# Optimization experiments

Hardware: AMD Instinct MI355X
Metric: run time of the kernel (lower is better)

Reference implementation:

```python
import jax, jax.numpy as jnp
import numpy as np

HID = 128
OUT = 1
L = 4
N_NODES = 50000
N_EDGES = 600000
NUM_GRAPHS = 256
ATOM_FEATS, ATOM_VOCAB = 9, 64
BOND_FEATS, BOND_VOCAB = 3, 8
BN_EPS = 1e-5


def setup_inputs() -> dict:
    key = jax.random.key(0)
    ks = jax.random.split(key, 16)
    x = jax.random.randint(ks[0], (N_NODES, ATOM_FEATS), 0, ATOM_VOCAB)
    edge_index = jax.random.randint(ks[1], (2, N_EDGES), 0, N_NODES)
    edge_attr = jax.random.randint(ks[2], (N_EDGES, BOND_FEATS), 0, BOND_VOCAB)
    batch = jnp.sort(jax.random.randint(ks[3], (N_NODES,), 0, NUM_GRAPHS))
    s = 0.05
    atom_emb = jax.random.normal(ks[4], (ATOM_FEATS, ATOM_VOCAB, HID), jnp.float32) * s
    bond_emb = jax.random.normal(ks[5], (BOND_FEATS, BOND_VOCAB, HID), jnp.float32) * s
    lin1_w = jax.random.normal(ks[6], (L, HID, HID), jnp.float32) * (1.0 / np.sqrt(HID))
    lin1_b = jnp.zeros((L, HID), jnp.float32)
    lin2_w = jax.random.normal(ks[7], (L, HID, HID), jnp.float32) * (1.0 / np.sqrt(HID))
    lin2_b = jnp.zeros((L, HID), jnp.float32)
    bn_gamma = jnp.ones((L, HID), jnp.float32)
    bn_beta = jnp.zeros((L, HID), jnp.float32)
    bn_mean = jax.random.normal(ks[8], (L, HID), jnp.float32) * 0.1
    bn_var = jax.random.uniform(ks[9], (L, HID), jnp.float32, 0.5, 1.5)
    mlp_w = jax.random.normal(ks[10], (HID, OUT), jnp.float32) * (1.0 / np.sqrt(HID))
    mlp_b = jnp.zeros((OUT,), jnp.float32)
    return dict(x=x, edge_index=edge_index, edge_attr=edge_attr, batch=batch,
                atom_emb=atom_emb, bond_emb=bond_emb,
                lin1_w=lin1_w, lin1_b=lin1_b, lin2_w=lin2_w, lin2_b=lin2_b,
                bn_gamma=bn_gamma, bn_beta=bn_beta, bn_mean=bn_mean, bn_var=bn_var,
                mlp_w=mlp_w, mlp_b=mlp_b)


def _multi_embed(tables, idx):
    # tables: [F, V, H], idx: [N, F] -> sum over F of tables[f][idx[:, f]] -> [N, H]
    return jax.vmap(lambda tab, i: tab[i], in_axes=(0, 1))(tables, idx).sum(0)


def reference(x, edge_index, edge_attr, batch, atom_emb, bond_emb,
              lin1_w, lin1_b, lin2_w, lin2_b, bn_gamma, bn_beta,
              bn_mean, bn_var, mlp_w, mlp_b):
    h = _multi_embed(atom_emb, x)            # [N, H]
    e = _multi_embed(bond_emb, edge_attr)    # [E, H]
    src, dst = edge_index[0], edge_index[1]
    for l in range(L):
        x_res = h
        # GINEConv (eps=0): MLP(x + sum_j ReLU(x_j + e_ji))
        msg = jax.nn.relu(h[src] + e)                          # [E, H]
        agg = jax.ops.segment_sum(msg, dst, num_segments=N_NODES)
        z = h + agg
        z = jax.nn.relu(z @ lin1_w[l] + lin1_b[l]) @ lin2_w[l] + lin2_b[l]
        # BatchNorm (eval: running stats)
        z = (z - bn_mean[l]) * (bn_gamma[l] / jnp.sqrt(bn_var[l] + BN_EPS)) + bn_beta[l]
        h = x_res + jax.nn.relu(z)
        # dropout is identity in eval mode
    sums = jax.ops.segment_sum(h, batch, num_segments=NUM_GRAPHS)
    cnt = jax.ops.segment_sum(jnp.ones((N_NODES, 1), h.dtype), batch, num_segments=NUM_GRAPHS)
    pooled = sums / jnp.maximum(cnt, 1.0)
    return pooled @ mlp_w + mlp_b
```

## Files before the change

kernel.cpp:

```cpp
#include <hip/hip_runtime.h>

#define NNODES 50000
#define NEDGES 600000
#define NGRAPH 256
#define HD     128
#define NLAYER 4
#define NBLK_SCAN 49

typedef __bf16 bf16;
typedef __attribute__((ext_vector_type(2))) __bf16 bf16x2;
typedef __attribute__((ext_vector_type(8))) __bf16 bf16x8;
typedef __attribute__((ext_vector_type(4))) float  f32x4;

#define CB_MLPW 0
#define CB_MLPB 128

#define PB_W    512
#define PB_BN   (PB_W + 2)
#define PB_MLP  (PB_BN + 1)
#define PB_ETAB (PB_MLP + 256)
#define PB_EMB  (PB_ETAB + 12500)
#define PB_HIST (PB_EMB + 2344)

struct PtrPack { const void* p[12]; };

__device__ __forceinline__ float ldf(const void* p, int i, int flag) {
    return flag ? (float)((const bf16*)p)[i] : ((const float*)p)[i];
}
__device__ __forceinline__ float blo(unsigned u) { return __uint_as_float(u << 16); }
__device__ __forceinline__ float bhi(unsigned u) { return __uint_as_float(u & 0xFFFF0000u); }

__global__ __launch_bounds__(256) void k_prep(PtrPack pk, const int* __restrict__ x,
                                              const int* __restrict__ ei,
                                              float* __restrict__ cvt, bf16* __restrict__ wtg,
                                              float* __restrict__ biasf, float* __restrict__ scalef,
                                              float* __restrict__ shiftf, bf16* __restrict__ etab,
                                              bf16* __restrict__ hbuf, int* __restrict__ deg) {
    const int flag = (((const unsigned*)pk.p[6])[0] != 0x3F800000u);
    int b = blockIdx.x, t = threadIdx.x;
    if (b < PB_W) {
        int idx = b * 256 + t;
        int mat = idx >> 14, rem = idx & 16383;
        int k = rem >> 7, n = rem & 127;
        const void* src = (mat < 4) ? pk.p[2] : pk.p[4];
        int mi = (mat < 4) ? mat : mat - 4;
        wtg[((size_t)mat << 14) + (n << 7) + k] = (bf16)ldf(src, (mi << 14) + (k << 7) + n, flag);
    } else if (b < PB_BN) {
        int i = (b - PB_W) * 256 + t;
        biasf[i] = ldf(pk.p[3], i, flag);
        float s = ldf(pk.p[6], i, flag) * rsqrtf(ldf(pk.p[9], i, flag) + 1e-5f);
        scalef[i] = s;
        shiftf[i] = (ldf(pk.p[5], i, flag) - ldf(pk.p[8], i, flag)) * s + ldf(pk.p[7], i, flag);
    } else if (b < PB_MLP) {
        if (t < 128)       cvt[CB_MLPW + t] = ldf(pk.p[10], t, flag);
        else if (t == 128) cvt[CB_MLPB] = ldf(pk.p[11], 0, flag);
    } else if (b < PB_ETAB) {
        int idx = (b - PB_MLP) * 256 + t;
        int combo = idx >> 7, ch = idx & 127;
        int c0 = combo & 7, c1 = (combo >> 3) & 7, c2 = combo >> 6;
        float v = ldf(pk.p[1], (c0 << 7) + ch, flag) +
                  ldf(pk.p[1], ((8 + c1) << 7) + ch, flag) +
                  ldf(pk.p[1], ((16 + c2) << 7) + ch, flag);
        etab[idx] = (bf16)v;
    } else if (b < PB_EMB) {
        int wid = t >> 6, lane = t & 63;
        int n = (b - PB_ETAB) * 4 + wid;
        if (n >= NNODES) return;
        const int* xr = x + n * 9;
        float ax = 0.f, ay = 0.f;
        if (flag) {
            const char* ae = (const char*)pk.p[0];
#pragma unroll
            for (int f = 0; f < 9; ++f) {
                int v = xr[f];
                unsigned hu = *(const unsigned*)(ae + (((size_t)(f * 64 + v)) << 8) + (lane << 2));
                ax += blo(hu); ay += bhi(hu);
            }
        } else {
            const float* ae = (const float*)pk.p[0];
#pragma unroll
            for (int f = 0; f < 9; ++f) {
                int v = xr[f];
                float2 tv = ((const float2*)(ae + (((size_t)(f * 64 + v)) << 7)))[lane];
                ax += tv.x; ay += tv.y;
            }
        }
        bf16x2 hv; hv[0] = (bf16)ax; hv[1] = (bf16)ay;
        ((bf16x2*)(hbuf + ((size_t)n << 7)))[lane] = hv;
    } else {
        int i = (b - PB_EMB) * 256 + t;
        if (i < NEDGES) atomicAdd(&deg[ei[NEDGES + i]], 1);
    }
}

__global__ void k_scan1(const int* __restrict__ deg, int* __restrict__ partials) {
    __shared__ int s[256];
    int t = threadIdx.x, b = blockIdx.x;
    int base = b * 1024 + t * 4;
    int sum = 0;
#pragma unroll
    for (int i = 0; i < 4; ++i) { int idx = base + i; if (idx < NNODES) sum += deg[idx]; }
    s[t] = sum; __syncthreads();
    for (int o = 128; o > 0; o >>= 1) { if (t < o) s[t] += s[t + o]; __syncthreads(); }
    if (t == 0) partials[b] = s[0];
}

__global__ void k_scan3(const int* __restrict__ deg, const int* __restrict__ partials,
                        int* __restrict__ row_start, int* __restrict__ cursor) {
    __shared__ int s[256];
    __shared__ int boff;
    int t = threadIdx.x, b = blockIdx.x;
    if (t < 64) {
        int own = (t < b && t < NBLK_SCAN) ? partials[t] : 0;
#pragma unroll
        for (int o = 32; o > 0; o >>= 1) own += __shfl_xor(own, o);
        if (t == 0) boff = own;
    }
    int base = b * 1024 + t * 4;
    int v[4]; int sum = 0;
#pragma unroll
    for (int i = 0; i < 4; ++i) {
        int idx = base + i;
        v[i] = (idx < NNODES) ? deg[idx] : 0;
        sum += v[i];
    }
    s[t] = sum; __syncthreads();
    for (int o = 1; o < 256; o <<= 1) {
        int add = (t >= o) ? s[t - o] : 0;
        __syncthreads();
        s[t] += add;
        __syncthreads();
    }
    int run = s[t] - sum + boff;
#pragma unroll
    for (int i = 0; i < 4; ++i) {
        int idx = base + i;
        if (idx < NNODES) { row_start[idx] = run; cursor[idx] = run; }
        run += v[i];
    }
    if (b == NBLK_SCAN - 1 && t == 255) row_start[NNODES] = run;
}

__global__ void k_fill(const int* __restrict__ ei, const int* __restrict__ ea,
                       int* __restrict__ cursor, unsigned* __restrict__ payload) {
    int i = blockIdx.x * 256 + threadIdx.x;
    if (i >= NEDGES) return;
    int dst = ei[NEDGES + i];
    int pos = atomicAdd(&cursor[dst], 1);
    unsigned p = (unsigned)ei[i] | ((unsigned)ea[3 * i] << 16) |
                 ((unsigned)ea[3 * i + 1] << 19) | ((unsigned)ea[3 * i + 2] << 22);
    payload[pos] = p;
}

__global__ __launch_bounds__(256) void k_agg(const bf16* __restrict__ hbuf,
                                             const bf16* __restrict__ etab,
                                             const int* __restrict__ row_start,
                                             const unsigned* __restrict__ payload,
                                             bf16* __restrict__ zbuf) {
    const int t = threadIdx.x;
    const int wid = t >> 6, lane = t & 63;
    const int quad = lane >> 4, l16 = lane & 15;
    const int n = blockIdx.x * 4 + wid;
    if (n >= NNODES) return;
    const int beg = row_start[n], end = row_start[n + 1];
    const char* hbp = (const char*)hbuf;
    const char* ebp = (const char*)etab;

    float acc[8];
#pragma unroll
    for (int k = 0; k < 8; ++k) acc[k] = 0.f;

    for (int base = beg; base < end; base += 32) {
        int m = end - base; if (m > 32) m = 32;
        unsigned pv = (base + lane < end) ? payload[base + lane] : 0u;
        for (int j = 0; j < m; j += 16) {
            unsigned pe[4]; uint4 he[4]; uint4 ee[4];
#pragma unroll
            for (int i = 0; i < 4; ++i) {
                int idx = j + i * 4 + quad;
                pe[i] = __shfl(pv, idx < m ? idx : 0);
            }
#pragma unroll
            for (int i = 0; i < 4; ++i) {
                he[i] = *(const uint4*)(hbp + (((size_t)(pe[i] & 0xFFFFu)) << 8) + (l16 << 4));
                ee[i] = *(const uint4*)(ebp + (((size_t)((pe[i] >> 16) & 511u)) << 8) + (l16 << 4));
            }
#pragma unroll
            for (int i = 0; i < 4; ++i) {
                bool ok = (j + i * 4 + quad) < m;
                float m0 = fmaxf(blo(he[i].x) + blo(ee[i].x), 0.f);
                float m1 = fmaxf(bhi(he[i].x) + bhi(ee[i].x), 0.f);
                float m2 = fmaxf(blo(he[i].y) + blo(ee[i].y), 0.f);
                float m3 = fmaxf(bhi(he[i].y) + bhi(ee[i].y), 0.f);
                float m4 = fmaxf(blo(he[i].z) + blo(ee[i].z), 0.f);
                float m5 = fmaxf(bhi(he[i].z) + bhi(ee[i].z), 0.f);
                float m6 = fmaxf(blo(he[i].w) + blo(ee[i].w), 0.f);
                float m7 = fmaxf(bhi(he[i].w) + bhi(ee[i].w), 0.f);
                if (ok) {
                    acc[0] += m0; acc[1] += m1; acc[2] += m2; acc[3] += m3;
                    acc[4] += m4; acc[5] += m5; acc[6] += m6; acc[7] += m7;
                }
            }
        }
    }

#pragma unroll
    for (int k = 0; k < 8; ++k) {
        acc[k] += __shfl_xor(acc[k], 16);
        acc[k] += __shfl_xor(acc[k], 32);
    }
    if (quad == 0) {
        uint4 hn = *(const uint4*)(hbp + ((size_t)n << 8) + (l16 << 4));
        bf16x8 z;
        z[0] = (bf16)(blo(hn.x) + acc[0]); z[1] = (bf16)(bhi(hn.x) + acc[1]);
        z[2] = (bf16)(blo(hn.y) + acc[2]); z[3] = (bf16)(bhi(hn.y) + acc[3]);
        z[4] = (bf16)(blo(hn.z) + acc[4]); z[5] = (bf16)(bhi(hn.z) + acc[5]);
        z[6] = (bf16)(blo(hn.w) + acc[6]); z[7] = (bf16)(bhi(hn.w) + acc[7]);
        *(bf16x8*)(zbuf + ((size_t)n << 7) + (l16 << 3)) = z;
    }
}

__global__ __launch_bounds__(256) void k_update(const bf16* __restrict__ zbuf,
                                                bf16* __restrict__ hbuf,
                                                const bf16* __restrict__ wtg,
                                                const float* __restrict__ biasf,
                                                const float* __restrict__ scalef,
                                                const float* __restrict__ shiftf,
                                                int layer) {
    __shared__ __align__(16) bf16 zs[64 * 128];
    __shared__ __align__(16) bf16 wt[128 * 128];
    const int t = threadIdx.x;
    const int w = t >> 6, lane = t & 63, r16 = lane & 15, q = lane >> 4;
    const int m0 = blockIdx.x * 64;

#pragma unroll
    for (int it = 0; it < 4; ++it) {
        int idx = t + it * 256;
        int r = idx >> 4, c = idx & 15;
        int row = m0 + r;
        bf16x8 v;
        if (row < NNODES) v = *(const bf16x8*)(zbuf + ((size_t)row << 7) + (c << 3));
        else { for (int ii = 0; ii < 8; ++ii) v[ii] = (bf16)0.0f; }
        *(bf16x8*)&zs[(r << 7) + ((c ^ (r & 7)) << 3)] = v;
    }
    {
        const bf16* w1 = wtg + ((size_t)layer << 14);
#pragma unroll
        for (int it = 0; it < 8; ++it) {
            int idx = t + it * 256;
            int r = idx >> 4, c = idx & 15;
            *(bf16x8*)&wt[(r << 7) + ((c ^ (r & 7)) << 3)] =
                *(const bf16x8*)(w1 + (r << 7) + (c << 3));
        }
    }
    bf16x8 w2r[8];
    {
        const bf16* w2 = wtg + ((size_t)(NLAYER + layer) << 14);
#pragma unroll
        for (int it = 0; it < 8; ++it) {
            int idx = t + it * 256;
            int r = idx >> 4, c = idx & 15;
            w2r[it] = *(const bf16x8*)(w2 + (r << 7) + (c << 3));
        }
    }
    __syncthreads();

    f32x4 acc[8];
#pragma unroll
    for (int j = 0; j < 8; ++j) acc[j] = (f32x4){0.f, 0.f, 0.f, 0.f};

    const int sw = r16 & 7;
#pragma unroll
    for (int kc = 0; kc < 4; ++kc) {
        int col = (((kc << 2) + q) ^ sw) << 3;
        bf16x8 a0 = *(const bf16x8*)&zs[((w * 16 + r16) << 7) + col];
        bf16x8 bb[8];
#pragma unroll
        for (int j = 0; j < 8; ++j) bb[j] = *(const bf16x8*)&wt[((j * 16 + r16) << 7) + col];
#pragma unroll
        for (int j = 0; j < 8; ++j)
            acc[j] = __builtin_amdgcn_mfma_f32_16x16x32_bf16(a0, bb[j], acc[j], 0, 0, 0);
    }
    {
        const float* b1 = biasf + (layer << 7);
#pragma unroll
        for (int j = 0; j < 8; ++j) {
            int n = j * 16 + r16;
            float bi = b1[n];
#pragma unroll
            for (int rg = 0; rg < 4; ++rg) {
                int row = w * 16 + q * 4 + rg;
                float v = fmaxf(acc[j][rg] + bi, 0.f);
                zs[(row << 7) + (((n >> 3) ^ (row & 7)) << 3) + (n & 7)] = (bf16)v;
            }
        }
    }
    __syncthreads();
#pragma unroll
    for (int it = 0; it < 8; ++it) {
        int idx = t + it * 256;
        int r = idx >> 4, c = idx & 15;
        *(bf16x8*)&wt[(r << 7) + ((c ^ (r & 7)) << 3)] = w2r[it];
    }
    __syncthreads();

#pragma unroll
    for (int j = 0; j < 8; ++j) acc[j] = (f32x4){0.f, 0.f, 0.f, 0.f};

#pragma unroll
    for (int kc = 0; kc < 4; ++kc) {
        int col = (((kc << 2) + q) ^ sw) << 3;
        bf16x8 a0 = *(const bf16x8*)&zs[((w * 16 + r16) << 7) + col];
        bf16x8 bb[8];
#pragma unroll
        for (int j = 0; j < 8; ++j) bb[j] = *(const bf16x8*)&wt[((j * 16 + r16) << 7) + col];
#pragma unroll
        for (int j = 0; j < 8; ++j)
            acc[j] = __builtin_amdgcn_mfma_f32_16x16x32_bf16(a0, bb[j], acc[j], 0, 0, 0);
    }
    {
        const float* sc = scalef + (layer << 7);
        const float* sh = shiftf + (layer << 7);
#pragma unroll
        for (int j = 0; j < 8; ++j) {
            int n = j * 16 + r16;
            float s_ = sc[n], h_ = sh[n];
#pragma unroll
            for (int rg = 0; rg < 4; ++rg) {
                int row = w * 16 + q * 4 + rg;
                float z = acc[j][rg] * s_ + h_;
                zs[(row << 7) + (((n >> 3) ^ (row & 7)) << 3) + (n & 7)] = (bf16)fmaxf(z, 0.f);
            }
        }
    }
    __syncthreads();
#pragma unroll
    for (int it = 0; it < 4; ++it) {
        int c = t + it * 256;
        int row = c >> 4, seg = c & 15;
        int grow = m0 + row;
        if (grow < NNODES) {
            bf16x8 zv = *(const bf16x8*)&zs[(row << 7) + ((seg ^ (row & 7)) << 3)];
            bf16* hp = hbuf + ((size_t)grow << 7) + (seg << 3);
            bf16x8 hv = *(const bf16x8*)hp;
            bf16x8 r;
#pragma unroll
            for (int k = 0; k < 8; ++k) r[k] = (bf16)((float)hv[k] + (float)zv[k]);
            *(bf16x8*)hp = r;
        }
    }
}

__global__ __launch_bounds__(256) void k_pool(const bf16* __restrict__ hbuf,
                                              const int* __restrict__ batch,
                                              const float* __restrict__ cvt,
                                              const unsigned* __restrict__ gam_raw,
                                              void* __restrict__ out) {
    const int flag = (*gam_raw != 0x3F800000u);
    int g = blockIdx.x;
    int t = threadIdx.x, wid = t >> 6, lane = t & 63;
    int lo = 0, hi = NNODES;
    while (lo < hi) { int m = (lo + hi) >> 1; if (batch[m] < g) lo = m + 1; else hi = m; }
    int s = lo;
    hi = NNODES;
    while (lo < hi) { int m = (lo + hi) >> 1; if (batch[m] <= g) lo = m + 1; else hi = m; }
    int e = lo;
    float ax = 0.f, ay = 0.f;
    for (int n = s + wid; n < e; n += 4) {
        unsigned hu = ((const unsigned*)(hbuf + ((size_t)n << 7)))[lane];
        ax += blo(hu);
        ay += bhi(hu);
    }
    __shared__ float red[4][128];
    red[wid][2 * lane] = ax;
    red[wid][2 * lane + 1] = ay;
    __syncthreads();
    __shared__ float fin[128];
    if (t < 128) {
        float sum = red[0][t] + red[1][t] + red[2][t] + red[3][t];
        float cnt = fmaxf((float)(e - s), 1.0f);
        fin[t] = (sum / cnt) * cvt[CB_MLPW + t];
    }
    __syncthreads();
    for (int o = 64; o > 0; o >>= 1) {
        if (t < o) fin[t] += fin[t + o];
        __syncthreads();
    }
    if (t == 0) {
        float r = fin[0] + cvt[CB_MLPB];
        if (flag) ((bf16*)out)[g] = (bf16)r;
        else      ((float*)out)[g] = r;
    }
}

extern "C" void kernel_launch(void* const* d_in, const int* in_sizes, int n_in,
                              void* d_out, int out_size, void* d_ws, size_t ws_size,
                              hipStream_t stream) {
    const int* x     = (const int*)d_in[0];
    const int* ei    = (const int*)d_in[1];
    const int* ea    = (const int*)d_in[2];
    const int* batch = (const int*)d_in[3];

    char* ws = (char*)d_ws;
    size_t o = 0;
    auto alloc = [&](size_t bytes) -> void* {
        void* p = ws + o;
        o = (o + bytes + 255) & ~(size_t)255;
        return p;
    };
    bf16*     hbuf      = (bf16*)alloc((size_t)NNODES * HD * 2);
    bf16*     zbuf      = (bf16*)alloc((size_t)NNODES * HD * 2);
    unsigned* payload   = (unsigned*)alloc((size_t)NEDGES * 4);
    int*      row_start = (int*)alloc((size_t)(NNODES + 1) * 4);
    int*      cursor    = (int*)alloc((size_t)NNODES * 4);
    int*      deg       = (int*)alloc((size_t)NNODES * 4);
    int*      partials  = (int*)alloc(64 * 4);
    bf16*     wtg       = (bf16*)alloc((size_t)8 * 128 * 128 * 2);
    bf16*     etab      = (bf16*)alloc((size_t)512 * 128 * 2);
    float*    cvt       = (float*)alloc((size_t)129 * 4);
    float*    biasf     = (float*)alloc(NLAYER * HD * 4);
    float*    scalef    = (float*)alloc(NLAYER * HD * 4);
    float*    shiftf    = (float*)alloc(NLAYER * HD * 4);

    PtrPack pk;
    for (int i = 0; i < 12; ++i) pk.p[i] = d_in[4 + i];
    const unsigned* gam_raw = (const unsigned*)d_in[10];

    hipMemsetAsync(deg, 0, (size_t)NNODES * 4, stream);
    k_prep<<<PB_HIST, 256, 0, stream>>>(pk, x, ei, cvt, wtg, biasf, scalef, shiftf, etab, hbuf, deg);
    k_scan1<<<NBLK_SCAN, 256, 0, stream>>>(deg, partials);
    k_scan3<<<NBLK_SCAN, 256, 0, stream>>>(deg, partials, row_start, cursor);
    k_fill<<<(NEDGES + 255) / 256, 256, 0, stream>>>(ei, ea, cursor, payload);
    for (int l = 0; l < NLAYER; ++l) {
        k_agg<<<(NNODES + 3) / 4, 256, 0, stream>>>(hbuf, etab, row_start, payload, zbuf);
        k_update<<<(NNODES + 63) / 64, 256, 0, stream>>>(zbuf, hbuf, wtg, biasf, scalef, shiftf, l);
    }
    k_pool<<<NGRAPH, 256, 0, stream>>>(hbuf, batch, cvt, gam_raw, d_out);
}
```

Baseline: 377.2 us.

## Split node features into four 32-channel planes for cache-local aggregation

Rearranges the hidden-state, z and edge-embedding buffers into four planes of 32 channels each, so every node row in a plane is 64 bytes. The aggregation kernel gets a second grid dimension that picks the plane, so each block gathers only one quarter of each neighbor row and the per-plane working set (about 3.2MB) can stay in cache. All producers and consumers (prep, update, pool) are changed to the new indexing. The cost is four times as many aggregation blocks, each re-reading the CSR payload, and narrower 4-byte gathers in place of 16-byte vector loads.

```diff
diff --git a/kernel.cpp b/kernel.cpp
--- a/kernel.cpp
+++ b/kernel.cpp
@@ -6,6 +6,10 @@
 #define HD     128
 #define NLAYER 4
 #define NBLK_SCAN 49
+
+#define PLANE_E  1600000
+#define PLANE_B  3200000
+#define ETAB_PLANE_E 16384
 
 typedef __bf16 bf16;
 typedef __attribute__((ext_vector_type(2))) __bf16 bf16x2;
@@ -61,7 +65,7 @@
         float v = ldf(pk.p[1], (c0 << 7) + ch, flag) +
                   ldf(pk.p[1], ((8 + c1) << 7) + ch, flag) +
                   ldf(pk.p[1], ((16 + c2) << 7) + ch, flag);
-        etab[idx] = (bf16)v;
+        etab[(ch >> 5) * ETAB_PLANE_E + combo * 32 + (ch & 31)] = (bf16)v;
     } else if (b < PB_EMB) {
         int wid = t >> 6, lane = t & 63;
         int n = (b - PB_ETAB) * 4 + wid;
@@ -85,8 +89,9 @@
                 ax += tv.x; ay += tv.y;
             }
         }
+        int ch = lane << 1;
         bf16x2 hv; hv[0] = (bf16)ax; hv[1] = (bf16)ay;
-        ((bf16x2*)(hbuf + ((size_t)n << 7)))[lane] = hv;
+        *(bf16x2*)(hbuf + (size_t)(ch >> 5) * PLANE_E + n * 32 + (ch & 31)) = hv;
     } else {
         int i = (b - PB_EMB) * 256 + t;
         if (i < NEDGES) atomicAdd(&deg[ei[NEDGES + i]], 1);
@@ -160,21 +165,20 @@
     const int t = threadIdx.x;
     const int wid = t >> 6, lane = t & 63;
     const int quad = lane >> 4, l16 = lane & 15;
+    const int plane = blockIdx.y;
     const int n = blockIdx.x * 4 + wid;
     if (n >= NNODES) return;
     const int beg = row_start[n], end = row_start[n + 1];
-    const char* hbp = (const char*)hbuf;
-    const char* ebp = (const char*)etab;
-
-    float acc[8];
-#pragma unroll
-    for (int k = 0; k < 8; ++k) acc[k] = 0.f;
+    const char* hbp = (const char*)hbuf + (size_t)plane * PLANE_B;
+    const char* ebp = (const char*)etab + (size_t)plane * (ETAB_PLANE_E * 2);
+
+    float a0 = 0.f, a1 = 0.f;
 
     for (int base = beg; base < end; base += 32) {
         int m = end - base; if (m > 32) m = 32;
         unsigned pv = (base + lane < end) ? payload[base + lane] : 0u;
         for (int j = 0; j < m; j += 16) {
-            unsigned pe[4]; uint4 he[4]; uint4 ee[4];
+            unsigned pe[4]; unsigned he[4]; unsigned ee[4];
 #pragma unroll
             for (int i = 0; i < 4; ++i) {
                 int idx = j + i * 4 + quad;
@@ -182,41 +186,27 @@
             }
 #pragma unroll
             for (int i = 0; i < 4; ++i) {
-                he[i] = *(const uint4*)(hbp + (((size_t)(pe[i] & 0xFFFFu)) << 8) + (l16 << 4));
-                ee[i] = *(const uint4*)(ebp + (((size_t)((pe[i] >> 16) & 511u)) << 8) + (l16 << 4));
+                he[i] = *(const unsigned*)(hbp + (((size_t)(pe[i] & 0xFFFFu)) << 6) + (l16 << 2));
+                ee[i] = *(const unsigned*)(ebp + (((size_t)((pe[i] >> 16) & 511u)) << 6) + (l16 << 2));
             }
 #pragma unroll
             for (int i = 0; i < 4; ++i) {
                 bool ok = (j + i * 4 + quad) < m;
-                float m0 = fmaxf(blo(he[i].x) + blo(ee[i].x), 0.f);
-                float m1 = fmaxf(bhi(he[i].x) + bhi(ee[i].x), 0.f);
-                float m2 = fmaxf(blo(he[i].y) + blo(ee[i].y), 0.f);
-                float m3 = fmaxf(bhi(he[i].y) + bhi(ee[i].y), 0.f);
-                float m4 = fmaxf(blo(he[i].z) + blo(ee[i].z), 0.f);
-                float m5 = fmaxf(bhi(he[i].z) + bhi(ee[i].z), 0.f);
-                float m6 = fmaxf(blo(he[i].w) + blo(ee[i].w), 0.f);
-                float m7 = fmaxf(bhi(he[i].w) + bhi(ee[i].w), 0.f);
-                if (ok) {
-                    acc[0] += m0; acc[1] += m1; acc[2] += m2; acc[3] += m3;
-                    acc[4] += m4; acc[5] += m5; acc[6] += m6; acc[7] += m7;
-                }
-            }
-        }
-    }
-
-#pragma unroll
-    for (int k = 0; k < 8; ++k) {
-        acc[k] += __shfl_xor(acc[k], 16);
-        acc[k] += __shfl_xor(acc[k], 32);
-    }
+                float m0 = fmaxf(blo(he[i]) + blo(ee[i]), 0.f);
+                float m1 = fmaxf(bhi(he[i]) + bhi(ee[i]), 0.f);
+                if (ok) { a0 += m0; a1 += m1; }
+            }
+        }
+    }
+
+    a0 += __shfl_xor(a0, 16); a0 += __shfl_xor(a0, 32);
+    a1 += __shfl_xor(a1, 16); a1 += __shfl_xor(a1, 32);
     if (quad == 0) {
-        uint4 hn = *(const uint4*)(hbp + ((size_t)n << 8) + (l16 << 4));
-        bf16x8 z;
-        z[0] = (bf16)(blo(hn.x) + acc[0]); z[1] = (bf16)(bhi(hn.x) + acc[1]);
-        z[2] = (bf16)(blo(hn.y) + acc[2]); z[3] = (bf16)(bhi(hn.y) + acc[3]);
-        z[4] = (bf16)(blo(hn.z) + acc[4]); z[5] = (bf16)(bhi(hn.z) + acc[5]);
-        z[6] = (bf16)(blo(hn.w) + acc[6]); z[7] = (bf16)(bhi(hn.w) + acc[7]);
-        *(bf16x8*)(zbuf + ((size_t)n << 7) + (l16 << 3)) = z;
+        unsigned hn = *(const unsigned*)(hbp + ((size_t)n << 6) + (l16 << 2));
+        bf16x2 z;
+        z[0] = (bf16)(blo(hn) + a0);
+        z[1] = (bf16)(bhi(hn) + a1);
+        *(bf16x2*)((char*)zbuf + (size_t)plane * PLANE_B + ((size_t)n << 6) + (l16 << 2)) = z;
     }
 }
 
@@ -239,7 +229,8 @@
         int r = idx >> 4, c = idx & 15;
         int row = m0 + r;
         bf16x8 v;
-        if (row < NNODES) v = *(const bf16x8*)(zbuf + ((size_t)row << 7) + (c << 3));
+        if (row < NNODES)
+            v = *(const bf16x8*)(zbuf + (size_t)(c >> 2) * PLANE_E + row * 32 + ((c & 3) << 3));
         else { for (int ii = 0; ii < 8; ++ii) v[ii] = (bf16)0.0f; }
         *(bf16x8*)&zs[(r << 7) + ((c ^ (r & 7)) << 3)] = v;
     }
@@ -336,12 +327,12 @@
     __syncthreads();
 #pragma unroll
     for (int it = 0; it < 4; ++it) {
-        int c = t + it * 256;
-        int row = c >> 4, seg = c & 15;
+        int c_ = t + it * 256;
+        int row = c_ >> 4, seg = c_ & 15;
         int grow = m0 + row;
         if (grow < NNODES) {
             bf16x8 zv = *(const bf16x8*)&zs[(row << 7) + ((seg ^ (row & 7)) << 3)];
-            bf16* hp = hbuf + ((size_t)grow << 7) + (seg << 3);
+            bf16* hp = hbuf + (size_t)(seg >> 2) * PLANE_E + grow * 32 + ((seg & 3) << 3);
             bf16x8 hv = *(const bf16x8*)hp;
             bf16x8 r;
 #pragma unroll
@@ -365,9 +356,10 @@
     hi = NNODES;
     while (lo < hi) { int m = (lo + hi) >> 1; if (batch[m] <= g) lo = m + 1; else hi = m; }
     int e = lo;
+    const char* hbp = (const char*)hbuf + (size_t)(lane >> 4) * PLANE_B;
     float ax = 0.f, ay = 0.f;
     for (int n = s + wid; n < e; n += 4) {
-        unsigned hu = ((const unsigned*)(hbuf + ((size_t)n << 7)))[lane];
+        unsigned hu = *(const unsigned*)(hbp + ((size_t)n << 6) + ((lane & 15) << 2));
         ax += blo(hu);
         ay += bhi(hu);
     }
@@ -431,8 +423,9 @@
     k_scan1<<<NBLK_SCAN, 256, 0, stream>>>(deg, partials);
     k_scan3<<<NBLK_SCAN, 256, 0, stream>>>(deg, partials, row_start, cursor);
     k_fill<<<(NEDGES + 255) / 256, 256, 0, stream>>>(ei, ea, cursor, payload);
+    dim3 agg_grid((NNODES + 3) / 4, 4);
     for (int l = 0; l < NLAYER; ++l) {
-        k_agg<<<(NNODES + 3) / 4, 256, 0, stream>>>(hbuf, etab, row_start, payload, zbuf);
+        k_agg<<<agg_grid, 256, 0, stream>>>(hbuf, etab, row_start, payload, zbuf);
         k_update<<<(NNODES + 63) / 64, 256, 0, stream>>>(zbuf, hbuf, wtg, biasf, scalef, shiftf, l);
     }
     k_pool<<<NGRAPH, 256, 0, stream>>>(hbuf, batch, cvt, gam_raw, d_out);
```

Result: slower. 493.1 us (+30.7%).
